# Kernel optimization log

Hardware: AMD Instinct MI355X
Metric: run time of the kernel (lower is better)

The kernel has to match this reference:

```python
import jax, jax.numpy as jnp
import numpy as np

B, T, HID = 2, 2048, 1024
H, D = 16, 64
ROPE = 32
GIDX = (2, 3, 4, 5)
MASK_VAL = -1e9


def setup_inputs() -> dict:
    key = jax.random.key(0)
    ks = jax.random.split(key, 5)
    x = jax.random.normal(ks[0], (B, T, HID), jnp.float32)
    mask = jnp.triu(jnp.ones((T, T), jnp.bool_), 1)  # True above diagonal -> masked (causal)
    qkv_w = jax.random.normal(ks[1], (3 * H * D, HID), jnp.float32) * (1.0 / np.sqrt(HID))
    qkv_b = jax.random.normal(ks[2], (3 * H * D,), jnp.float32) * 0.02
    out_w = jax.random.normal(ks[3], (HID, H * D), jnp.float32) * (1.0 / np.sqrt(H * D))
    out_b = jax.random.normal(ks[4], (HID,), jnp.float32) * 0.02
    return {"x": x, "mask": mask, "qkv_w": qkv_w, "qkv_b": qkv_b, "out_w": out_w, "out_b": out_b}


def _rope_tables(t):
    inv_freq = 1.0 / (10000.0 ** (jnp.arange(0, ROPE, 2, dtype=jnp.float32) / ROPE))
    freqs = jnp.arange(t, dtype=jnp.float32)[:, None] * inv_freq[None, :]  # [T, ROPE/2]
    return jnp.cos(freqs), jnp.sin(freqs)


def _apply_rotary(x, cos, sin):
    # x: [B,H,T,D]; rotate first ROPE dims as interleaved pairs
    xr = x[..., :ROPE].reshape(*x.shape[:-1], ROPE // 2, 2)
    x1, x2 = xr[..., 0], xr[..., 1]
    rot = jnp.stack([x1 * cos - x2 * sin, x1 * sin + x2 * cos], axis=-1).reshape(*x.shape[:-1], ROPE)
    return jnp.concatenate([rot, x[..., ROPE:]], axis=-1)


def reference(x, mask, qkv_w, qkv_b, out_w, out_b):
    b, t, _ = x.shape
    qkv = x @ qkv_w.T + qkv_b                      # [B,T,3*H*D]
    q, k, v = jnp.split(qkv, 3, axis=-1)
    q, k, v = [y.reshape(b, t, H, D).transpose(0, 2, 1, 3) for y in (q, k, v)]  # [B,H,T,D]
    cos, sin = _rope_tables(t)                      # [T, ROPE/2] broadcast over B,H
    q = _apply_rotary(q, cos, sin)
    k = _apply_rotary(k, cos, sin)
    scale = 1.0 / np.sqrt(D)
    # local dense causal attention
    scores = jnp.einsum('bhqd,bhkd->bhqk', q, k) * scale
    scores = jnp.where(mask, MASK_VAL, scores)
    out_local = jnp.einsum('bhqk,bhkd->bhqd', jax.nn.softmax(scores, axis=-1), v)
    # global token pass with its own causal overlay
    gidx = jnp.array(GIDX)
    gq = q[:, :, gidx]                              # [B,H,G,D]
    gs = jnp.einsum('bhgd,bhkd->bhgk', gq, k) * scale
    gmask = jnp.arange(t)[None, :] > gidx[:, None]  # [G,T]: col > row -> masked
    gs = jnp.where(gmask, MASK_VAL, gs)
    gout = jnp.einsum('bhgk,bhkd->bhgd', jax.nn.softmax(gs, axis=-1), v)
    out = out_local.at[:, :, gidx].set(gout)
    attn_out = out.transpose(0, 2, 1, 3).reshape(b, t, H * D)
    return attn_out @ out_w.T + out_b
```

## Files before the change

### kernel.cpp

```cpp
#include <hip/hip_runtime.h>
#include <math.h>

typedef unsigned short u16;
typedef unsigned int u32;
typedef __attribute__((ext_vector_type(4))) float f32x4;
typedef __attribute__((ext_vector_type(8))) short bf16x8;

#define B_ 2
#define T_ 2048
#define H_ 16
#define HID 1024
#define NQKV 3072
#define M_ 4096
#define SCALE_Q 0.18033688011112042f

__device__ __forceinline__ u16 f2bf(float f) {
  union { float f; unsigned u; } v; v.f = f;
  unsigned r = v.u + 0x7FFFu + ((v.u >> 16) & 1u);
  return (u16)(r >> 16);
}
__device__ __forceinline__ float bf2f(u16 u) {
  union { unsigned u; float f; } v; v.u = ((unsigned)u) << 16; return v.f;
}
__device__ __forceinline__ u32 cvt_pk_bf16(float lo, float hi) {
  u32 r;
  asm("v_cvt_pk_bf16_f32 %0, %1, %2" : "=v"(r) : "v"(lo), "v"(hi));
  return r;
}
__device__ __forceinline__ float fexp2(float x) { return __builtin_amdgcn_exp2f(x); }

__device__ __forceinline__ void gload16(const void* g, void* l) {
  __builtin_amdgcn_global_load_lds((const __attribute__((address_space(1))) void*)g,
                                   (__attribute__((address_space(3))) void*)l, 16, 0, 0);
}

__global__ void prep(const float* __restrict__ x, const float* __restrict__ qkv_w,
                     const float* __restrict__ out_w, u16* __restrict__ xb,
                     u16* __restrict__ wqkv, u16* __restrict__ wout, float* __restrict__ tab) {
  int bid = blockIdx.x;
  if (bid < 128) {
    int i = bid * 256 + threadIdx.x;
    int tpos = i >> 4, f = i & 15;
    float ang = (float)tpos * exp2f(-(float)f * 0.83048202372184058696f);
    float s, c;
    sincosf(ang, &s, &c);
    tab[i * 2] = c;
    tab[i * 2 + 1] = s;
    return;
  }
  bid -= 128;
  const float* in;
  u16* out;
  if (bid < 4096) { in = x; out = xb; }
  else if (bid < 7168) { bid -= 4096; in = qkv_w; out = wqkv; }
  else { bid -= 7168; in = out_w; out = wout; }
  int i = bid * 256 + threadIdx.x;
  float4 v = ((const float4*)in)[i];
  uint2 o;
  o.x = (unsigned)f2bf(v.x) | ((unsigned)f2bf(v.y) << 16);
  o.y = (unsigned)f2bf(v.z) | ((unsigned)f2bf(v.w) << 16);
  ((uint2*)out)[i] = o;
}

template<int BM, int WROWS, int OUT_BF16>
__global__ __launch_bounds__(256) void gemm_nt(const u16* __restrict__ A,
    const u16* __restrict__ Bt, const float* __restrict__ bias,
    void* __restrict__ outp, int N, int K)
{
  constexpr int WCOLS = 4 / WROWS;
  constexpr int MI = BM / WROWS / 16;
  constexpr int NI = 128 / WCOLS / 16;
  __shared__ u16 lsA[2][BM * 32];
  __shared__ u16 lsB[2][128 * 32];
  const int t = threadIdx.x;
  const int l = t & 63, w = t >> 6;
  const int wm = (w / WCOLS) * (BM / WROWS);
  const int wn = (w % WCOLS) * (128 / WCOLS);
  const int lr = l & 15, lg = l >> 4;
  const long bm = (long)blockIdx.y * BM, bn = (long)blockIdx.x * 128;

  f32x4 acc[MI][NI];
#pragma unroll
  for (int i = 0; i < MI; i++)
#pragma unroll
    for (int j = 0; j < NI; j++) acc[i][j] = (f32x4){0.f, 0.f, 0.f, 0.f};

  const int srow = l >> 2, sko = (l & 3) * 8;
  const u16* Ab = A + (bm + srow) * (long)K + sko;
  const u16* Bb = Bt + (bn + srow) * (long)K + sko;

  auto stage = [&](int buf, int k0) {
    gload16(Ab + (long)(w * 16) * K + k0, &lsA[buf][w * 512]);
    if constexpr (BM == 128)
      gload16(Ab + (long)((w + 4) * 16) * K + k0, &lsA[buf][(w + 4) * 512]);
    gload16(Bb + (long)(w * 16) * K + k0, &lsB[buf][w * 512]);
    gload16(Bb + (long)((w + 4) * 16) * K + k0, &lsB[buf][(w + 4) * 512]);
  };

  stage(0, 0);
  __syncthreads();
  int cur = 0;
  for (int k0 = 0; k0 < K; k0 += 32) {
    if (k0 + 32 < K) stage(cur ^ 1, k0 + 32);
    bf16x8 af[MI], bfv[NI];
#pragma unroll
    for (int mi = 0; mi < MI; mi++)
      af[mi] = *(const bf16x8*)&lsA[cur][(wm + mi * 16 + lr) * 32 + lg * 8];
#pragma unroll
    for (int ni = 0; ni < NI; ni++)
      bfv[ni] = *(const bf16x8*)&lsB[cur][(wn + ni * 16 + lr) * 32 + lg * 8];
    __builtin_amdgcn_s_setprio(1);
#pragma unroll
    for (int mi = 0; mi < MI; mi++)
#pragma unroll
      for (int ni = 0; ni < NI; ni++)
        acc[mi][ni] = __builtin_amdgcn_mfma_f32_16x16x32_bf16(af[mi], bfv[ni], acc[mi][ni], 0, 0, 0);
    __builtin_amdgcn_s_setprio(0);
    __syncthreads();
    cur ^= 1;
  }
#pragma unroll
  for (int mi = 0; mi < MI; mi++)
#pragma unroll
    for (int ni = 0; ni < NI; ni++) {
      long row = bm + wm + mi * 16 + lg * 4;
      long col = bn + wn + ni * 16 + lr;
      float bv = bias[col];
#pragma unroll
      for (int r = 0; r < 4; r++) {
        float v = acc[mi][ni][r] + bv;
        if (OUT_BF16) ((u16*)outp)[(row + r) * (long)N + col] = f2bf(v);
        else          ((float*)outp)[(row + r) * (long)N + col] = v;
      }
    }
}

__global__ __launch_bounds__(256) void post_qkv(const u16* __restrict__ qkv,
    const float* __restrict__ tab, u16* __restrict__ Q, u16* __restrict__ K,
    u16* __restrict__ Vt) {
  __shared__ u16 ls[64 * 72];
  const int bid = blockIdx.x;
  if (bid < 256) {
    int idx = bid * 256 + threadIdx.x;
    int h = idx & 15;
    int m = idx >> 4;
    int tpos = m & (T_ - 1);
    int b = m >> 11;
    const u16* qr = qkv + (long)m * NQKV + h * 64;
    alignas(16) u16 qv[64];
    alignas(16) u16 kv[64];
#pragma unroll
    for (int c = 0; c < 8; c++) {
      *(int4*)&qv[c * 8] = *(const int4*)&qr[c * 8];
      *(int4*)&kv[c * 8] = *(const int4*)&qr[1024 + c * 8];
    }
#pragma unroll
    for (int i = 0; i < 16; i++) {
      float c = tab[(tpos * 16 + i) * 2];
      float s = tab[(tpos * 16 + i) * 2 + 1];
      float q1 = bf2f(qv[2 * i]), q2 = bf2f(qv[2 * i + 1]);
      qv[2 * i]     = f2bf((q1 * c - q2 * s) * SCALE_Q);
      qv[2 * i + 1] = f2bf((q1 * s + q2 * c) * SCALE_Q);
      float k1 = bf2f(kv[2 * i]), k2 = bf2f(kv[2 * i + 1]);
      kv[2 * i]     = f2bf(k1 * c - k2 * s);
      kv[2 * i + 1] = f2bf(k1 * s + k2 * c);
    }
#pragma unroll
    for (int j = 32; j < 64; j++) qv[j] = f2bf(bf2f(qv[j]) * SCALE_Q);
    long ob = ((long)(b * 16 + h) * T_ + tpos) * 64;
#pragma unroll
    for (int c = 0; c < 8; c++) {
      *(int4*)&Q[ob + c * 8] = *(int4*)&qv[c * 8];
      *(int4*)&K[ob + c * 8] = *(int4*)&kv[c * 8];
    }
  } else {
    int id2 = bid - 256;
    int tt = id2 & 31, bh = id2 >> 5;
    int b = bh >> 4, h = bh & 15;
    int t = threadIdx.x;
    for (int c = t; c < 512; c += 256) {
      int row = c >> 3, off = (c & 7) * 8;
      *(int4*)&ls[row * 72 + off] =
          *(const int4*)&qkv[((long)(b * T_ + tt * 64 + row)) * NQKV + 2048 + h * 64 + off];
    }
    __syncthreads();
    for (int c = t; c < 512; c += 256) {
      int d = c >> 3, toff = (c & 7) * 8;
      alignas(16) u16 tmp[8];
#pragma unroll
      for (int j = 0; j < 8; j++) tmp[j] = ls[(toff + j) * 72 + d];
      *(int4*)&Vt[((long)(bh * 64 + d)) * T_ + tt * 64 + toff] = *(int4*)tmp;
    }
  }
}

__global__ __launch_bounds__(256, 4) void fattn(const u16* __restrict__ Q, const u16* __restrict__ Kp,
                                                const u16* __restrict__ V, u16* __restrict__ O) {
  const int id = blockIdx.x;
  const int qt = 31 - (id >> 5);
  const int bh = id & 31;
  __shared__ u16 lsK[2][64 * 64];
  __shared__ u16 lsV[2][64 * 64];
  __shared__ u32 lsP[4][16 * 36];
  const int t = threadIdx.x, l = t & 63, w = t >> 6;
  const int lr = l & 15, lg = l >> 4;
  const u16* Qb = Q + (long)bh * T_ * 64;
  const u16* Kb = Kp + (long)bh * T_ * 64;
  const u16* Vb = V + (long)bh * 64 * T_;
  u32* lsPw = lsP[w];

  bf16x8 aq[2];
#pragma unroll
  for (int ks = 0; ks < 2; ks++)
    aq[ks] = *(const bf16x8*)&Qb[((long)(qt * 64 + w * 16 + lr)) * 64 + ks * 32 + lg * 8];

  f32x4 o[4];
#pragma unroll
  for (int di = 0; di < 4; di++) o[di] = (f32x4){0.f, 0.f, 0.f, 0.f};
  float mrow = -1e30f, lrow = 0.f;

  const int srow = l >> 3;
  const int scx = ((l & 7) ^ srow) * 8;
  const long kgo0 = (long)(16 * w + srow) * 64 + scx;
  const long kgo1 = (long)(16 * w + 8 + srow) * 64 + scx;
  const long vgo0 = (long)(16 * w + srow) * T_ + scx;
  const long vgo1 = (long)(16 * w + 8 + srow) * T_ + scx;

  gload16(Kb + kgo0, &lsK[0][(2 * w) * 512]);
  gload16(Kb + kgo1, &lsK[0][(2 * w + 1) * 512]);
  gload16(Vb + vgo0, &lsV[0][(2 * w) * 512]);
  gload16(Vb + vgo1, &lsV[0][(2 * w + 1) * 512]);
  __syncthreads();

  int cur = 0;
  for (int kt = 0; kt <= qt; kt++) {
    if (kt < qt) {
      const u16* kp = Kb + (kt + 1) * 4096;
      const u16* vp = Vb + (kt + 1) * 64;
      gload16(kp + kgo0, &lsK[cur ^ 1][(2 * w) * 512]);
      gload16(kp + kgo1, &lsK[cur ^ 1][(2 * w + 1) * 512]);
      gload16(vp + vgo0, &lsV[cur ^ 1][(2 * w) * 512]);
      gload16(vp + vgo1, &lsV[cur ^ 1][(2 * w + 1) * 512]);
    }

    f32x4 s[4];
#pragma unroll
    for (int ji = 0; ji < 4; ji++) s[ji] = (f32x4){0.f, 0.f, 0.f, 0.f};
    __builtin_amdgcn_s_setprio(1);
#pragma unroll
    for (int ks = 0; ks < 2; ks++)
#pragma unroll
      for (int ji = 0; ji < 4; ji++) {
        int row = ji * 16 + lr;
        bf16x8 kf = *(const bf16x8*)&lsK[cur][row * 64 + ((ks * 32 + lg * 8) ^ ((row & 7) * 8))];
        s[ji] = __builtin_amdgcn_mfma_f32_16x16x32_bf16(kf, aq[ks], s[ji], 0, 0, 0);
      }
    __builtin_amdgcn_s_setprio(0);

    if (kt == qt) {
      int qloc = w * 16 + lr;
#pragma unroll
      for (int ji = 0; ji < 4; ji++)
#pragma unroll
        for (int r = 0; r < 4; r++)
          if (ji * 16 + lg * 4 + r > qloc) s[ji][r] = -1e30f;
    }

    float mx = s[0][0];
#pragma unroll
    for (int ji = 0; ji < 4; ji++)
#pragma unroll
      for (int r = 0; r < 4; r++) mx = fmaxf(mx, s[ji][r]);
    mx = fmaxf(mx, __shfl_xor(mx, 16, 64));
    mx = fmaxf(mx, __shfl_xor(mx, 32, 64));

    if (__any(mx - mrow > 8.f)) {
      float newm = fmaxf(mrow, mx);
      float sf = fexp2(mrow - newm);
      mrow = newm;
      lrow *= sf;
#pragma unroll
      for (int r = 0; r < 4; r++) {
        float sfb = __shfl(sf, lg * 4 + r, 64);
#pragma unroll
        for (int di = 0; di < 4; di++) o[di][r] *= sfb;
      }
    }

    float rs = 0.f;
    u32 pd[8];
#pragma unroll
    for (int ji = 0; ji < 4; ji++)
#pragma unroll
      for (int hh = 0; hh < 2; hh++) {
        float p0 = fexp2(s[ji][2 * hh] - mrow);
        float p1 = fexp2(s[ji][2 * hh + 1] - mrow);
        rs += p0 + p1;
        pd[ji * 2 + hh] = cvt_pk_bf16(p0, p1);
      }
    rs += __shfl_xor(rs, 16, 64);
    rs += __shfl_xor(rs, 32, 64);
    lrow += rs;

#pragma unroll
    for (int ji = 0; ji < 4; ji++)
      *(uint2*)&lsPw[lr * 36 + ji * 8 + lg * 2] = make_uint2(pd[2 * ji], pd[2 * ji + 1]);
    __builtin_amdgcn_s_setprio(1);
#pragma unroll
    for (int js = 0; js < 2; js++) {
      bf16x8 pa = *(const bf16x8*)&lsPw[lr * 36 + js * 16 + lg * 4];
#pragma unroll
      for (int di = 0; di < 4; di++) {
        int drow = di * 16 + lr;
        bf16x8 vb = *(const bf16x8*)&lsV[cur][drow * 64 + ((js * 32 + lg * 8) ^ ((drow & 7) * 8))];
        o[di] = __builtin_amdgcn_mfma_f32_16x16x32_bf16(pa, vb, o[di], 0, 0, 0);
      }
    }
    __builtin_amdgcn_s_setprio(0);

    if (kt < qt) __syncthreads();
    cur ^= 1;
  }

  const int b = bh >> 4, h = bh & 15;
  float inv = 1.f / lrow;
#pragma unroll
  for (int r = 0; r < 4; r++) {
    float invb = __shfl(inv, lg * 4 + r, 64);
#pragma unroll
    for (int di = 0; di < 4; di++) {
      long rowt = (long)(b * T_ + qt * 64 + w * 16 + lg * 4 + r);
      O[rowt * 1024 + h * 64 + di * 16 + lr] = f2bf(o[di][r] * invb);
    }
  }
}

extern "C" void kernel_launch(void* const* d_in, const int* in_sizes, int n_in,
                              void* d_out, int out_size, void* d_ws, size_t ws_size,
                              hipStream_t stream) {
  (void)in_sizes; (void)n_in; (void)out_size; (void)ws_size;
  const float* x     = (const float*)d_in[0];
  const float* qkv_w = (const float*)d_in[2];
  const float* qkv_b = (const float*)d_in[3];
  const float* out_w = (const float*)d_in[4];
  const float* out_b = (const float*)d_in[5];
  char* ws = (char*)d_ws;
  size_t off = 0;
  auto alloc = [&](size_t n) { void* p = ws + off; off += (n + 255) & ~(size_t)255; return p; };
  u16*   xb    = (u16*)alloc((size_t)M_ * HID * 2);
  u16*   wqkv  = (u16*)alloc((size_t)NQKV * HID * 2);
  u16*   wout  = (u16*)alloc((size_t)HID * HID * 2);
  u16*   qkvb  = (u16*)alloc((size_t)M_ * NQKV * 2);
  u16*   Qb    = (u16*)alloc((size_t)M_ * HID * 2);
  u16*   Kb    = (u16*)alloc((size_t)M_ * HID * 2);
  u16*   Vtb   = (u16*)alloc((size_t)M_ * HID * 2);
  u16*   attnb = (u16*)alloc((size_t)M_ * HID * 2);
  float* tab   = (float*)alloc((size_t)T_ * 16 * 2 * 4);

  prep<<<8320, 256, 0, stream>>>(x, qkv_w, out_w, xb, wqkv, wout, tab);
  gemm_nt<128, 2, 1><<<dim3(NQKV / 128, M_ / 128), 256, 0, stream>>>(xb, wqkv, qkv_b, qkvb, NQKV, HID);
  post_qkv<<<1280, 256, 0, stream>>>(qkvb, tab, Qb, Kb, Vtb);
  fattn<<<1024, 256, 0, stream>>>(Qb, Kb, Vtb, attnb);
  gemm_nt<64, 1, 0><<<dim3(HID / 128, M_ / 64), 256, 0, stream>>>(attnb, wout, out_b, (float*)d_out, HID, HID);
}
```

Before: 210.7 us.

## Enlarge attention query tile to 128 rows with 8 waves and parametrize GEMM BK

The flash-attention kernel now launches 512-thread blocks, each covering 128 query rows with 8 waves. The waves share each 64-row K/V tile loaded into LDS, which halves the K/V global traffic per query row. Waves whose rows lie entirely before a key tile skip its compute, and the max and sum reductions become tree-shaped. The GEMM gains a BK template parameter: the output projection uses BK=64 with a 128-row tile, cutting barriers per K step, while the QKV GEMM is unchanged. The risks are fewer attention blocks (512) and more causal imbalance inside a block, plus higher LDS and register use.

```diff
diff --git a/kernel.cpp b/kernel.cpp
--- a/kernel.cpp
+++ b/kernel.cpp
@@ -62,7 +62,7 @@
   ((uint2*)out)[i] = o;
 }
 
-template<int BM, int WROWS, int OUT_BF16>
+template<int BM, int BK, int WROWS, int OUT_BF16>
 __global__ __launch_bounds__(256) void gemm_nt(const u16* __restrict__ A,
     const u16* __restrict__ Bt, const float* __restrict__ bias,
     void* __restrict__ outp, int N, int K)
@@ -70,8 +70,11 @@
   constexpr int WCOLS = 4 / WROWS;
   constexpr int MI = BM / WROWS / 16;
   constexpr int NI = 128 / WCOLS / 16;
-  __shared__ u16 lsA[2][BM * 32];
-  __shared__ u16 lsB[2][128 * 32];
+  constexpr int RPG = 512 / BK;
+  constexpr int GA = BM / RPG / 4;
+  constexpr int GB = 128 / RPG / 4;
+  __shared__ u16 lsA[2][BM * BK];
+  __shared__ u16 lsB[2][128 * BK];
   const int t = threadIdx.x;
   const int l = t & 63, w = t >> 6;
   const int wm = (w / WCOLS) * (BM / WROWS);
@@ -85,36 +88,41 @@
 #pragma unroll
     for (int j = 0; j < NI; j++) acc[i][j] = (f32x4){0.f, 0.f, 0.f, 0.f};
 
-  const int srow = l >> 2, sko = (l & 3) * 8;
+  const int srow = l / (BK / 8);
+  const int sko = (l % (BK / 8)) * 8;
   const u16* Ab = A + (bm + srow) * (long)K + sko;
   const u16* Bb = Bt + (bn + srow) * (long)K + sko;
 
   auto stage = [&](int buf, int k0) {
-    gload16(Ab + (long)(w * 16) * K + k0, &lsA[buf][w * 512]);
-    if constexpr (BM == 128)
-      gload16(Ab + (long)((w + 4) * 16) * K + k0, &lsA[buf][(w + 4) * 512]);
-    gload16(Bb + (long)(w * 16) * K + k0, &lsB[buf][w * 512]);
-    gload16(Bb + (long)((w + 4) * 16) * K + k0, &lsB[buf][(w + 4) * 512]);
+#pragma unroll
+    for (int g = 0; g < GA; g++)
+      gload16(Ab + (long)((w * GA + g) * RPG) * K + k0, &lsA[buf][(w * GA + g) * 512]);
+#pragma unroll
+    for (int g = 0; g < GB; g++)
+      gload16(Bb + (long)((w * GB + g) * RPG) * K + k0, &lsB[buf][(w * GB + g) * 512]);
   };
 
   stage(0, 0);
   __syncthreads();
   int cur = 0;
-  for (int k0 = 0; k0 < K; k0 += 32) {
-    if (k0 + 32 < K) stage(cur ^ 1, k0 + 32);
-    bf16x8 af[MI], bfv[NI];
-#pragma unroll
-    for (int mi = 0; mi < MI; mi++)
-      af[mi] = *(const bf16x8*)&lsA[cur][(wm + mi * 16 + lr) * 32 + lg * 8];
-#pragma unroll
-    for (int ni = 0; ni < NI; ni++)
-      bfv[ni] = *(const bf16x8*)&lsB[cur][(wn + ni * 16 + lr) * 32 + lg * 8];
+  for (int k0 = 0; k0 < K; k0 += BK) {
+    if (k0 + BK < K) stage(cur ^ 1, k0 + BK);
     __builtin_amdgcn_s_setprio(1);
 #pragma unroll
-    for (int mi = 0; mi < MI; mi++)
+    for (int kb = 0; kb < BK / 32; kb++) {
+      bf16x8 af[MI], bfv[NI];
+#pragma unroll
+      for (int mi = 0; mi < MI; mi++)
+        af[mi] = *(const bf16x8*)&lsA[cur][(wm + mi * 16 + lr) * BK + kb * 32 + lg * 8];
 #pragma unroll
       for (int ni = 0; ni < NI; ni++)
-        acc[mi][ni] = __builtin_amdgcn_mfma_f32_16x16x32_bf16(af[mi], bfv[ni], acc[mi][ni], 0, 0, 0);
+        bfv[ni] = *(const bf16x8*)&lsB[cur][(wn + ni * 16 + lr) * BK + kb * 32 + lg * 8];
+#pragma unroll
+      for (int mi = 0; mi < MI; mi++)
+#pragma unroll
+        for (int ni = 0; ni < NI; ni++)
+          acc[mi][ni] = __builtin_amdgcn_mfma_f32_16x16x32_bf16(af[mi], bfv[ni], acc[mi][ni], 0, 0, 0);
+    }
     __builtin_amdgcn_s_setprio(0);
     __syncthreads();
     cur ^= 1;
@@ -194,25 +202,27 @@
   }
 }
 
-__global__ __launch_bounds__(256, 4) void fattn(const u16* __restrict__ Q, const u16* __restrict__ Kp,
+__global__ __launch_bounds__(512, 4) void fattn(const u16* __restrict__ Q, const u16* __restrict__ Kp,
                                                 const u16* __restrict__ V, u16* __restrict__ O) {
   const int id = blockIdx.x;
-  const int qt = 31 - (id >> 5);
+  const int qs = 15 - (id >> 5);
   const int bh = id & 31;
   __shared__ u16 lsK[2][64 * 64];
   __shared__ u16 lsV[2][64 * 64];
-  __shared__ u32 lsP[4][16 * 36];
+  __shared__ u32 lsP[8][16 * 36];
   const int t = threadIdx.x, l = t & 63, w = t >> 6;
   const int lr = l & 15, lg = l >> 4;
   const u16* Qb = Q + (long)bh * T_ * 64;
   const u16* Kb = Kp + (long)bh * T_ * 64;
   const u16* Vb = V + (long)bh * 64 * T_;
   u32* lsPw = lsP[w];
+  const int qbase = qs * 128 + w * 16;
+  const int qg = qbase + lr;
 
   bf16x8 aq[2];
 #pragma unroll
   for (int ks = 0; ks < 2; ks++)
-    aq[ks] = *(const bf16x8*)&Qb[((long)(qt * 64 + w * 16 + lr)) * 64 + ks * 32 + lg * 8];
+    aq[ks] = *(const bf16x8*)&Qb[(long)qg * 64 + ks * 32 + lg * 8];
 
   f32x4 o[4];
 #pragma unroll
@@ -221,104 +231,103 @@
 
   const int srow = l >> 3;
   const int scx = ((l & 7) ^ srow) * 8;
-  const long kgo0 = (long)(16 * w + srow) * 64 + scx;
-  const long kgo1 = (long)(16 * w + 8 + srow) * 64 + scx;
-  const long vgo0 = (long)(16 * w + srow) * T_ + scx;
-  const long vgo1 = (long)(16 * w + 8 + srow) * T_ + scx;
-
-  gload16(Kb + kgo0, &lsK[0][(2 * w) * 512]);
-  gload16(Kb + kgo1, &lsK[0][(2 * w + 1) * 512]);
-  gload16(Vb + vgo0, &lsV[0][(2 * w) * 512]);
-  gload16(Vb + vgo1, &lsV[0][(2 * w + 1) * 512]);
+  const long kgo = (long)(8 * w + srow) * 64 + scx;
+  const long vgo = (long)(8 * w + srow) * T_ + scx;
+
+  gload16(Kb + kgo, &lsK[0][w * 512]);
+  gload16(Vb + vgo, &lsV[0][w * 512]);
   __syncthreads();
 
   int cur = 0;
-  for (int kt = 0; kt <= qt; kt++) {
-    if (kt < qt) {
-      const u16* kp = Kb + (kt + 1) * 4096;
-      const u16* vp = Vb + (kt + 1) * 64;
-      gload16(kp + kgo0, &lsK[cur ^ 1][(2 * w) * 512]);
-      gload16(kp + kgo1, &lsK[cur ^ 1][(2 * w + 1) * 512]);
-      gload16(vp + vgo0, &lsV[cur ^ 1][(2 * w) * 512]);
-      gload16(vp + vgo1, &lsV[cur ^ 1][(2 * w + 1) * 512]);
-    }
-
-    f32x4 s[4];
-#pragma unroll
-    for (int ji = 0; ji < 4; ji++) s[ji] = (f32x4){0.f, 0.f, 0.f, 0.f};
-    __builtin_amdgcn_s_setprio(1);
-#pragma unroll
-    for (int ks = 0; ks < 2; ks++)
-#pragma unroll
-      for (int ji = 0; ji < 4; ji++) {
-        int row = ji * 16 + lr;
-        bf16x8 kf = *(const bf16x8*)&lsK[cur][row * 64 + ((ks * 32 + lg * 8) ^ ((row & 7) * 8))];
-        s[ji] = __builtin_amdgcn_mfma_f32_16x16x32_bf16(kf, aq[ks], s[ji], 0, 0, 0);
-      }
-    __builtin_amdgcn_s_setprio(0);
-
-    if (kt == qt) {
-      int qloc = w * 16 + lr;
+  const int ktmax = 2 * qs + 1;
+  for (int kt = 0; kt <= ktmax; kt++) {
+    if (kt < ktmax) {
+      gload16(Kb + (long)(kt + 1) * 4096 + kgo, &lsK[cur ^ 1][w * 512]);
+      gload16(Vb + (long)(kt + 1) * 64 + vgo, &lsV[cur ^ 1][w * 512]);
+    }
+    const int kbase = kt * 64;
+    if (kbase <= qbase + 15) {
+      f32x4 s[4];
+#pragma unroll
+      for (int ji = 0; ji < 4; ji++) s[ji] = (f32x4){0.f, 0.f, 0.f, 0.f};
+      __builtin_amdgcn_s_setprio(1);
+#pragma unroll
+      for (int ks = 0; ks < 2; ks++)
+#pragma unroll
+        for (int ji = 0; ji < 4; ji++) {
+          int row = ji * 16 + lr;
+          bf16x8 kf = *(const bf16x8*)&lsK[cur][row * 64 + ((ks * 32 + lg * 8) ^ ((row & 7) * 8))];
+          s[ji] = __builtin_amdgcn_mfma_f32_16x16x32_bf16(kf, aq[ks], s[ji], 0, 0, 0);
+        }
+      __builtin_amdgcn_s_setprio(0);
+
+      if (kbase + 63 > qbase) {
+#pragma unroll
+        for (int ji = 0; ji < 4; ji++)
+#pragma unroll
+          for (int r = 0; r < 4; r++)
+            if (kbase + ji * 16 + lg * 4 + r > qg) s[ji][r] = -1e30f;
+      }
+
+      float m01 = fmaxf(fmaxf(s[0][0], s[0][1]), fmaxf(s[0][2], s[0][3]));
+      float m23 = fmaxf(fmaxf(s[1][0], s[1][1]), fmaxf(s[1][2], s[1][3]));
+      float m45 = fmaxf(fmaxf(s[2][0], s[2][1]), fmaxf(s[2][2], s[2][3]));
+      float m67 = fmaxf(fmaxf(s[3][0], s[3][1]), fmaxf(s[3][2], s[3][3]));
+      float mx = fmaxf(fmaxf(m01, m23), fmaxf(m45, m67));
+      mx = fmaxf(mx, __shfl_xor(mx, 16, 64));
+      mx = fmaxf(mx, __shfl_xor(mx, 32, 64));
+
+      if (__any(mx - mrow > 8.f)) {
+        float newm = fmaxf(mrow, mx);
+        float sf = fexp2(mrow - newm);
+        mrow = newm;
+        lrow *= sf;
+#pragma unroll
+        for (int r = 0; r < 4; r++) {
+          float sfb = __shfl(sf, lg * 4 + r, 64);
+#pragma unroll
+          for (int di = 0; di < 4; di++) o[di][r] *= sfb;
+        }
+      }
+
+      float p[16];
+      u32 pd[8];
 #pragma unroll
       for (int ji = 0; ji < 4; ji++)
 #pragma unroll
-        for (int r = 0; r < 4; r++)
-          if (ji * 16 + lg * 4 + r > qloc) s[ji][r] = -1e30f;
-    }
-
-    float mx = s[0][0];
-#pragma unroll
-    for (int ji = 0; ji < 4; ji++)
-#pragma unroll
-      for (int r = 0; r < 4; r++) mx = fmaxf(mx, s[ji][r]);
-    mx = fmaxf(mx, __shfl_xor(mx, 16, 64));
-    mx = fmaxf(mx, __shfl_xor(mx, 32, 64));
-
-    if (__any(mx - mrow > 8.f)) {
-      float newm = fmaxf(mrow, mx);
-      float sf = fexp2(mrow - newm);
-      mrow = newm;
-      lrow *= sf;
-#pragma unroll
-      for (int r = 0; r < 4; r++) {
-        float sfb = __shfl(sf, lg * 4 + r, 64);
-#pragma unroll
-        for (int di = 0; di < 4; di++) o[di][r] *= sfb;
-      }
-    }
-
-    float rs = 0.f;
-    u32 pd[8];
-#pragma unroll
-    for (int ji = 0; ji < 4; ji++)
-#pragma unroll
-      for (int hh = 0; hh < 2; hh++) {
-        float p0 = fexp2(s[ji][2 * hh] - mrow);
-        float p1 = fexp2(s[ji][2 * hh + 1] - mrow);
-        rs += p0 + p1;
-        pd[ji * 2 + hh] = cvt_pk_bf16(p0, p1);
-      }
-    rs += __shfl_xor(rs, 16, 64);
-    rs += __shfl_xor(rs, 32, 64);
-    lrow += rs;
-
-#pragma unroll
-    for (int ji = 0; ji < 4; ji++)
-      *(uint2*)&lsPw[lr * 36 + ji * 8 + lg * 2] = make_uint2(pd[2 * ji], pd[2 * ji + 1]);
-    __builtin_amdgcn_s_setprio(1);
-#pragma unroll
-    for (int js = 0; js < 2; js++) {
-      bf16x8 pa = *(const bf16x8*)&lsPw[lr * 36 + js * 16 + lg * 4];
-#pragma unroll
-      for (int di = 0; di < 4; di++) {
-        int drow = di * 16 + lr;
-        bf16x8 vb = *(const bf16x8*)&lsV[cur][drow * 64 + ((js * 32 + lg * 8) ^ ((drow & 7) * 8))];
-        o[di] = __builtin_amdgcn_mfma_f32_16x16x32_bf16(pa, vb, o[di], 0, 0, 0);
-      }
-    }
-    __builtin_amdgcn_s_setprio(0);
-
-    if (kt < qt) __syncthreads();
+        for (int r = 0; r < 4; r++) p[ji * 4 + r] = fexp2(s[ji][r] - mrow);
+#pragma unroll
+      for (int jj = 0; jj < 8; jj++) pd[jj] = cvt_pk_bf16(p[2 * jj], p[2 * jj + 1]);
+      float rs = 0.f;
+      {
+        float a0 = (p[0] + p[1]) + (p[2] + p[3]);
+        float a1 = (p[4] + p[5]) + (p[6] + p[7]);
+        float a2 = (p[8] + p[9]) + (p[10] + p[11]);
+        float a3 = (p[12] + p[13]) + (p[14] + p[15]);
+        rs = (a0 + a1) + (a2 + a3);
+      }
+      rs += __shfl_xor(rs, 16, 64);
+      rs += __shfl_xor(rs, 32, 64);
+      lrow += rs;
+
+#pragma unroll
+      for (int ji = 0; ji < 4; ji++)
+        *(uint2*)&lsPw[lr * 36 + ji * 8 + lg * 2] = make_uint2(pd[2 * ji], pd[2 * ji + 1]);
+      __builtin_amdgcn_s_setprio(1);
+#pragma unroll
+      for (int js = 0; js < 2; js++) {
+        bf16x8 pa = *(const bf16x8*)&lsPw[lr * 36 + js * 16 + lg * 4];
+#pragma unroll
+        for (int di = 0; di < 4; di++) {
+          int drow = di * 16 + lr;
+          bf16x8 vb = *(const bf16x8*)&lsV[cur][drow * 64 + ((js * 32 + lg * 8) ^ ((drow & 7) * 8))];
+          o[di] = __builtin_amdgcn_mfma_f32_16x16x32_bf16(pa, vb, o[di], 0, 0, 0);
+        }
+      }
+      __builtin_amdgcn_s_setprio(0);
+    }
+
+    if (kt < ktmax) __syncthreads();
     cur ^= 1;
   }
 
@@ -329,7 +338,7 @@
     float invb = __shfl(inv, lg * 4 + r, 64);
 #pragma unroll
     for (int di = 0; di < 4; di++) {
-      long rowt = (long)(b * T_ + qt * 64 + w * 16 + lg * 4 + r);
+      long rowt = (long)(b * T_ + qbase + lg * 4 + r);
       O[rowt * 1024 + h * 64 + di * 16 + lr] = f2bf(o[di][r] * invb);
     }
   }
@@ -358,8 +367,8 @@
   float* tab   = (float*)alloc((size_t)T_ * 16 * 2 * 4);
 
   prep<<<8320, 256, 0, stream>>>(x, qkv_w, out_w, xb, wqkv, wout, tab);
-  gemm_nt<128, 2, 1><<<dim3(NQKV / 128, M_ / 128), 256, 0, stream>>>(xb, wqkv, qkv_b, qkvb, NQKV, HID);
+  gemm_nt<128, 32, 2, 1><<<dim3(NQKV / 128, M_ / 128), 256, 0, stream>>>(xb, wqkv, qkv_b, qkvb, NQKV, HID);
   post_qkv<<<1280, 256, 0, stream>>>(qkvb, tab, Qb, Kb, Vtb);
-  fattn<<<1024, 256, 0, stream>>>(Qb, Kb, Vtb, attnb);
-  gemm_nt<64, 1, 0><<<dim3(HID / 128, M_ / 64), 256, 0, stream>>>(attnb, wout, out_b, (float*)d_out, HID, HID);
-}
+  fattn<<<512, 512, 0, stream>>>(Qb, Kb, Vtb, attnb);
+  gemm_nt<128, 64, 2, 0><<<dim3(HID / 128, M_ / 128), 256, 0, stream>>>(attnb, wout, out_b, (float*)d_out, HID, HID);
+}
```

Measured after the change: 220.5 us. 4.6% more time.

## Double query rows per attention wave and enlarge QKV GEMM tile

Applied to the files above, without the earlier changes.

The flash attention kernel now gives each wave 32 query rows (two 16-row groups) over a 128-row query block. Each K/V tile loaded into shared memory therefore feeds twice as many MFMAs, and the grid is halved. Fully masked key tiles are skipped per wave, and occupancy is lowered to 3 blocks. Separately, the QKV GEMM uses a 256-row M tile with generalized staging loops and launch bounds of 2, which raises register pressure and reduces block count.

```diff
diff --git a/kernel.cpp b/kernel.cpp
--- a/kernel.cpp
+++ b/kernel.cpp
@@ -63,13 +63,15 @@
 }
 
 template<int BM, int WROWS, int OUT_BF16>
-__global__ __launch_bounds__(256) void gemm_nt(const u16* __restrict__ A,
+__global__ __launch_bounds__(256, 2) void gemm_nt(const u16* __restrict__ A,
     const u16* __restrict__ Bt, const float* __restrict__ bias,
     void* __restrict__ outp, int N, int K)
 {
   constexpr int WCOLS = 4 / WROWS;
   constexpr int MI = BM / WROWS / 16;
   constexpr int NI = 128 / WCOLS / 16;
+  constexpr int GA = BM / 16 / 4;
+  constexpr int GB = 128 / 16 / 4;
   __shared__ u16 lsA[2][BM * 32];
   __shared__ u16 lsB[2][128 * 32];
   const int t = threadIdx.x;
@@ -90,11 +92,12 @@
   const u16* Bb = Bt + (bn + srow) * (long)K + sko;
 
   auto stage = [&](int buf, int k0) {
-    gload16(Ab + (long)(w * 16) * K + k0, &lsA[buf][w * 512]);
-    if constexpr (BM == 128)
-      gload16(Ab + (long)((w + 4) * 16) * K + k0, &lsA[buf][(w + 4) * 512]);
-    gload16(Bb + (long)(w * 16) * K + k0, &lsB[buf][w * 512]);
-    gload16(Bb + (long)((w + 4) * 16) * K + k0, &lsB[buf][(w + 4) * 512]);
+#pragma unroll
+    for (int g = 0; g < GA; g++)
+      gload16(Ab + (long)((w * GA + g) * 16) * K + k0, &lsA[buf][(w * GA + g) * 512]);
+#pragma unroll
+    for (int g = 0; g < GB; g++)
+      gload16(Bb + (long)((w * GB + g) * 16) * K + k0, &lsB[buf][(w * GB + g) * 512]);
   };
 
   stage(0, 0);
@@ -194,30 +197,35 @@
   }
 }
 
-__global__ __launch_bounds__(256, 4) void fattn(const u16* __restrict__ Q, const u16* __restrict__ Kp,
+__global__ __launch_bounds__(256, 3) void fattn(const u16* __restrict__ Q, const u16* __restrict__ Kp,
                                                 const u16* __restrict__ V, u16* __restrict__ O) {
   const int id = blockIdx.x;
-  const int qt = 31 - (id >> 5);
+  const int qs = 15 - (id >> 5);
   const int bh = id & 31;
   __shared__ u16 lsK[2][64 * 64];
   __shared__ u16 lsV[2][64 * 64];
-  __shared__ u32 lsP[4][16 * 36];
+  __shared__ u32 lsP[4][32 * 36];
   const int t = threadIdx.x, l = t & 63, w = t >> 6;
   const int lr = l & 15, lg = l >> 4;
   const u16* Qb = Q + (long)bh * T_ * 64;
   const u16* Kb = Kp + (long)bh * T_ * 64;
   const u16* Vb = V + (long)bh * 64 * T_;
   u32* lsPw = lsP[w];
-
-  bf16x8 aq[2];
-#pragma unroll
-  for (int ks = 0; ks < 2; ks++)
-    aq[ks] = *(const bf16x8*)&Qb[((long)(qt * 64 + w * 16 + lr)) * 64 + ks * 32 + lg * 8];
-
-  f32x4 o[4];
-#pragma unroll
-  for (int di = 0; di < 4; di++) o[di] = (f32x4){0.f, 0.f, 0.f, 0.f};
-  float mrow = -1e30f, lrow = 0.f;
+  const int qbase = qs * 128 + w * 32;
+
+  bf16x8 aq[2][2];
+#pragma unroll
+  for (int qg = 0; qg < 2; qg++)
+#pragma unroll
+    for (int ks = 0; ks < 2; ks++)
+      aq[qg][ks] = *(const bf16x8*)&Qb[((long)(qbase + qg * 16 + lr)) * 64 + ks * 32 + lg * 8];
+
+  f32x4 o[2][4];
+#pragma unroll
+  for (int qg = 0; qg < 2; qg++)
+#pragma unroll
+    for (int di = 0; di < 4; di++) o[qg][di] = (f32x4){0.f, 0.f, 0.f, 0.f};
+  float mrow[2] = {-1e30f, -1e30f}, lrow[2] = {0.f, 0.f};
 
   const int srow = l >> 3;
   const int scx = ((l & 7) ^ srow) * 8;
@@ -233,8 +241,9 @@
   __syncthreads();
 
   int cur = 0;
-  for (int kt = 0; kt <= qt; kt++) {
-    if (kt < qt) {
+  const int ktmax = 2 * qs + 1;
+  for (int kt = 0; kt <= ktmax; kt++) {
+    if (kt < ktmax) {
       const u16* kp = Kb + (kt + 1) * 4096;
       const u16* vp = Vb + (kt + 1) * 64;
       gload16(kp + kgo0, &lsK[cur ^ 1][(2 * w) * 512]);
@@ -242,95 +251,114 @@
       gload16(vp + vgo0, &lsV[cur ^ 1][(2 * w) * 512]);
       gload16(vp + vgo1, &lsV[cur ^ 1][(2 * w + 1) * 512]);
     }
-
-    f32x4 s[4];
-#pragma unroll
-    for (int ji = 0; ji < 4; ji++) s[ji] = (f32x4){0.f, 0.f, 0.f, 0.f};
-    __builtin_amdgcn_s_setprio(1);
-#pragma unroll
-    for (int ks = 0; ks < 2; ks++)
-#pragma unroll
-      for (int ji = 0; ji < 4; ji++) {
-        int row = ji * 16 + lr;
-        bf16x8 kf = *(const bf16x8*)&lsK[cur][row * 64 + ((ks * 32 + lg * 8) ^ ((row & 7) * 8))];
-        s[ji] = __builtin_amdgcn_mfma_f32_16x16x32_bf16(kf, aq[ks], s[ji], 0, 0, 0);
+    const int kbase = kt * 64;
+    if (kbase <= qbase + 31) {
+      f32x4 s[2][4];
+#pragma unroll
+      for (int qg = 0; qg < 2; qg++)
+#pragma unroll
+        for (int ji = 0; ji < 4; ji++) s[qg][ji] = (f32x4){0.f, 0.f, 0.f, 0.f};
+      __builtin_amdgcn_s_setprio(1);
+#pragma unroll
+      for (int ks = 0; ks < 2; ks++)
+#pragma unroll
+        for (int ji = 0; ji < 4; ji++) {
+          int row = ji * 16 + lr;
+          bf16x8 kf = *(const bf16x8*)&lsK[cur][row * 64 + ((ks * 32 + lg * 8) ^ ((row & 7) * 8))];
+          s[0][ji] = __builtin_amdgcn_mfma_f32_16x16x32_bf16(kf, aq[0][ks], s[0][ji], 0, 0, 0);
+          s[1][ji] = __builtin_amdgcn_mfma_f32_16x16x32_bf16(kf, aq[1][ks], s[1][ji], 0, 0, 0);
+        }
+      __builtin_amdgcn_s_setprio(0);
+
+#pragma unroll
+      for (int qg = 0; qg < 2; qg++) {
+        const int qg_q = qbase + qg * 16 + lr;
+        if (kbase + 63 > qbase + qg * 16) {
+#pragma unroll
+          for (int ji = 0; ji < 4; ji++)
+#pragma unroll
+            for (int r = 0; r < 4; r++)
+              if (kbase + ji * 16 + lg * 4 + r > qg_q) s[qg][ji][r] = -1e30f;
+        }
+
+        float m01 = fmaxf(fmaxf(s[qg][0][0], s[qg][0][1]), fmaxf(s[qg][0][2], s[qg][0][3]));
+        float m23 = fmaxf(fmaxf(s[qg][1][0], s[qg][1][1]), fmaxf(s[qg][1][2], s[qg][1][3]));
+        float m45 = fmaxf(fmaxf(s[qg][2][0], s[qg][2][1]), fmaxf(s[qg][2][2], s[qg][2][3]));
+        float m67 = fmaxf(fmaxf(s[qg][3][0], s[qg][3][1]), fmaxf(s[qg][3][2], s[qg][3][3]));
+        float mx = fmaxf(fmaxf(m01, m23), fmaxf(m45, m67));
+        mx = fmaxf(mx, __shfl_xor(mx, 16, 64));
+        mx = fmaxf(mx, __shfl_xor(mx, 32, 64));
+
+        if (__any(mx - mrow[qg] > 8.f)) {
+          float newm = fmaxf(mrow[qg], mx);
+          float sf = fexp2(mrow[qg] - newm);
+          mrow[qg] = newm;
+          lrow[qg] *= sf;
+#pragma unroll
+          for (int r = 0; r < 4; r++) {
+            float sfb = __shfl(sf, lg * 4 + r, 64);
+#pragma unroll
+            for (int di = 0; di < 4; di++) o[qg][di][r] *= sfb;
+          }
+        }
+
+        float p[16];
+        u32 pd[8];
+#pragma unroll
+        for (int ji = 0; ji < 4; ji++)
+#pragma unroll
+          for (int r = 0; r < 4; r++) p[ji * 4 + r] = fexp2(s[qg][ji][r] - mrow[qg]);
+#pragma unroll
+        for (int jj = 0; jj < 8; jj++) pd[jj] = cvt_pk_bf16(p[2 * jj], p[2 * jj + 1]);
+        float rs;
+        {
+          float a0 = (p[0] + p[1]) + (p[2] + p[3]);
+          float a1 = (p[4] + p[5]) + (p[6] + p[7]);
+          float a2 = (p[8] + p[9]) + (p[10] + p[11]);
+          float a3 = (p[12] + p[13]) + (p[14] + p[15]);
+          rs = (a0 + a1) + (a2 + a3);
+        }
+        rs += __shfl_xor(rs, 16, 64);
+        rs += __shfl_xor(rs, 32, 64);
+        lrow[qg] += rs;
+
+#pragma unroll
+        for (int ji = 0; ji < 4; ji++)
+          *(uint2*)&lsPw[(qg * 16 + lr) * 36 + ji * 8 + lg * 2] = make_uint2(pd[2 * ji], pd[2 * ji + 1]);
       }
-    __builtin_amdgcn_s_setprio(0);
-
-    if (kt == qt) {
-      int qloc = w * 16 + lr;
-#pragma unroll
-      for (int ji = 0; ji < 4; ji++)
-#pragma unroll
-        for (int r = 0; r < 4; r++)
-          if (ji * 16 + lg * 4 + r > qloc) s[ji][r] = -1e30f;
-    }
-
-    float mx = s[0][0];
-#pragma unroll
-    for (int ji = 0; ji < 4; ji++)
-#pragma unroll
-      for (int r = 0; r < 4; r++) mx = fmaxf(mx, s[ji][r]);
-    mx = fmaxf(mx, __shfl_xor(mx, 16, 64));
-    mx = fmaxf(mx, __shfl_xor(mx, 32, 64));
-
-    if (__any(mx - mrow > 8.f)) {
-      float newm = fmaxf(mrow, mx);
-      float sf = fexp2(mrow - newm);
-      mrow = newm;
-      lrow *= sf;
-#pragma unroll
-      for (int r = 0; r < 4; r++) {
-        float sfb = __shfl(sf, lg * 4 + r, 64);
-#pragma unroll
-        for (int di = 0; di < 4; di++) o[di][r] *= sfb;
+
+      __builtin_amdgcn_s_setprio(1);
+#pragma unroll
+      for (int js = 0; js < 2; js++) {
+        bf16x8 pa0 = *(const bf16x8*)&lsPw[lr * 36 + js * 16 + lg * 4];
+        bf16x8 pa1 = *(const bf16x8*)&lsPw[(16 + lr) * 36 + js * 16 + lg * 4];
+#pragma unroll
+        for (int di = 0; di < 4; di++) {
+          int drow = di * 16 + lr;
+          bf16x8 vb = *(const bf16x8*)&lsV[cur][drow * 64 + ((js * 32 + lg * 8) ^ ((drow & 7) * 8))];
+          o[0][di] = __builtin_amdgcn_mfma_f32_16x16x32_bf16(pa0, vb, o[0][di], 0, 0, 0);
+          o[1][di] = __builtin_amdgcn_mfma_f32_16x16x32_bf16(pa1, vb, o[1][di], 0, 0, 0);
+        }
       }
-    }
-
-    float rs = 0.f;
-    u32 pd[8];
-#pragma unroll
-    for (int ji = 0; ji < 4; ji++)
-#pragma unroll
-      for (int hh = 0; hh < 2; hh++) {
-        float p0 = fexp2(s[ji][2 * hh] - mrow);
-        float p1 = fexp2(s[ji][2 * hh + 1] - mrow);
-        rs += p0 + p1;
-        pd[ji * 2 + hh] = cvt_pk_bf16(p0, p1);
+      __builtin_amdgcn_s_setprio(0);
+    }
+
+    if (kt < ktmax) __syncthreads();
+    cur ^= 1;
+  }
+
+  const int b = bh >> 4, h = bh & 15;
+#pragma unroll
+  for (int qg = 0; qg < 2; qg++) {
+    float inv = 1.f / lrow[qg];
+#pragma unroll
+    for (int r = 0; r < 4; r++) {
+      float invb = __shfl(inv, lg * 4 + r, 64);
+#pragma unroll
+      for (int di = 0; di < 4; di++) {
+        long rowt = (long)(b * T_ + qbase + qg * 16 + lg * 4 + r);
+        O[rowt * 1024 + h * 64 + di * 16 + lr] = f2bf(o[qg][di][r] * invb);
       }
-    rs += __shfl_xor(rs, 16, 64);
-    rs += __shfl_xor(rs, 32, 64);
-    lrow += rs;
-
-#pragma unroll
-    for (int ji = 0; ji < 4; ji++)
-      *(uint2*)&lsPw[lr * 36 + ji * 8 + lg * 2] = make_uint2(pd[2 * ji], pd[2 * ji + 1]);
-    __builtin_amdgcn_s_setprio(1);
-#pragma unroll
-    for (int js = 0; js < 2; js++) {
-      bf16x8 pa = *(const bf16x8*)&lsPw[lr * 36 + js * 16 + lg * 4];
-#pragma unroll
-      for (int di = 0; di < 4; di++) {
-        int drow = di * 16 + lr;
-        bf16x8 vb = *(const bf16x8*)&lsV[cur][drow * 64 + ((js * 32 + lg * 8) ^ ((drow & 7) * 8))];
-        o[di] = __builtin_amdgcn_mfma_f32_16x16x32_bf16(pa, vb, o[di], 0, 0, 0);
-      }
-    }
-    __builtin_amdgcn_s_setprio(0);
-
-    if (kt < qt) __syncthreads();
-    cur ^= 1;
-  }
-
-  const int b = bh >> 4, h = bh & 15;
-  float inv = 1.f / lrow;
-#pragma unroll
-  for (int r = 0; r < 4; r++) {
-    float invb = __shfl(inv, lg * 4 + r, 64);
-#pragma unroll
-    for (int di = 0; di < 4; di++) {
-      long rowt = (long)(b * T_ + qt * 64 + w * 16 + lg * 4 + r);
-      O[rowt * 1024 + h * 64 + di * 16 + lr] = f2bf(o[di][r] * invb);
     }
   }
 }
@@ -358,8 +386,8 @@
   float* tab   = (float*)alloc((size_t)T_ * 16 * 2 * 4);
 
   prep<<<8320, 256, 0, stream>>>(x, qkv_w, out_w, xb, wqkv, wout, tab);
-  gemm_nt<128, 2, 1><<<dim3(NQKV / 128, M_ / 128), 256, 0, stream>>>(xb, wqkv, qkv_b, qkvb, NQKV, HID);
+  gemm_nt<256, 2, 1><<<dim3(NQKV / 128, M_ / 256), 256, 0, stream>>>(xb, wqkv, qkv_b, qkvb, NQKV, HID);
   post_qkv<<<1280, 256, 0, stream>>>(qkvb, tab, Qb, Kb, Vtb);
-  fattn<<<1024, 256, 0, stream>>>(Qb, Kb, Vtb, attnb);
+  fattn<<<512, 256, 0, stream>>>(Qb, Kb, Vtb, attnb);
   gemm_nt<64, 1, 0><<<dim3(HID / 128, M_ / 64), 256, 0, stream>>>(attnb, wout, out_b, (float*)d_out, HID, HID);
 }
```

Result: slower. 229.0 us (+8.7%).

## Fuse RoPE, Q scaling and head-split/V-transpose into QKV GEMM epilogue

Applied to the files above, without the earlier changes.

The QKV GEMM epilogue now applies bias, rotary embedding (pairing lanes through a shuffle), the Q scale and the per-head layout scatter itself. It writes Q, K and transposed V directly and drops the intermediate qkv buffer and the post_qkv kernel. This removes one kernel launch and a full round trip of the 4096x3072 bf16 intermediate through global memory. In exchange the epilogue stores are scattered 2-byte writes for Q/K and strided 8-byte writes for V, where the removed kernel used 16-byte vector stores. The output GEMM is specialized into a non-templated kernel with the same tiling.

```diff
diff --git a/kernel.cpp b/kernel.cpp
--- a/kernel.cpp
+++ b/kernel.cpp
@@ -62,20 +62,118 @@
   ((uint2*)out)[i] = o;
 }
 
-template<int BM, int WROWS, int OUT_BF16>
-__global__ __launch_bounds__(256) void gemm_nt(const u16* __restrict__ A,
+__global__ __launch_bounds__(256) void gemm_qkv(const u16* __restrict__ A,
+    const u16* __restrict__ Bt, const float* __restrict__ bias, const float* __restrict__ tab,
+    u16* __restrict__ Q, u16* __restrict__ K, u16* __restrict__ Vt)
+{
+  __shared__ u16 lsA[2][128 * 32];
+  __shared__ u16 lsB[2][128 * 32];
+  const int t = threadIdx.x;
+  const int l = t & 63, w = t >> 6;
+  const int wm = (w >> 1) * 64, wn = (w & 1) * 64;
+  const int lr = l & 15, lg = l >> 4;
+  const long bm = (long)blockIdx.y * 128, bn = (long)blockIdx.x * 128;
+  const int KD = HID;
+
+  f32x4 acc[4][4];
+#pragma unroll
+  for (int i = 0; i < 4; i++)
+#pragma unroll
+    for (int j = 0; j < 4; j++) acc[i][j] = (f32x4){0.f, 0.f, 0.f, 0.f};
+
+  const int srow = l >> 2, sko = (l & 3) * 8;
+  const u16* Ab = A + (bm + srow) * (long)KD + sko;
+  const u16* Bb = Bt + (bn + srow) * (long)KD + sko;
+
+  auto stage = [&](int buf, int k0) {
+#pragma unroll
+    for (int g = 0; g < 2; g++)
+      gload16(Ab + (long)((w * 2 + g) * 16) * KD + k0, &lsA[buf][(w * 2 + g) * 512]);
+#pragma unroll
+    for (int g = 0; g < 2; g++)
+      gload16(Bb + (long)((w * 2 + g) * 16) * KD + k0, &lsB[buf][(w * 2 + g) * 512]);
+  };
+
+  stage(0, 0);
+  __syncthreads();
+  int cur = 0;
+  for (int k0 = 0; k0 < KD; k0 += 32) {
+    if (k0 + 32 < KD) stage(cur ^ 1, k0 + 32);
+    bf16x8 af[4], bfv[4];
+#pragma unroll
+    for (int mi = 0; mi < 4; mi++)
+      af[mi] = *(const bf16x8*)&lsA[cur][(wm + mi * 16 + lr) * 32 + lg * 8];
+#pragma unroll
+    for (int ni = 0; ni < 4; ni++)
+      bfv[ni] = *(const bf16x8*)&lsB[cur][(wn + ni * 16 + lr) * 32 + lg * 8];
+    __builtin_amdgcn_s_setprio(1);
+#pragma unroll
+    for (int mi = 0; mi < 4; mi++)
+#pragma unroll
+      for (int ni = 0; ni < 4; ni++)
+        acc[mi][ni] = __builtin_amdgcn_mfma_f32_16x16x32_bf16(af[mi], bfv[ni], acc[mi][ni], 0, 0, 0);
+    __builtin_amdgcn_s_setprio(0);
+    __syncthreads();
+    cur ^= 1;
+  }
+
+  const int region = (int)(bn >> 10);
+  const int h = (int)(((bn + wn) & 1023) >> 6);
+  const float2* tab2 = (const float2*)tab;
+  u16* QK = (region == 0) ? Q : K;
+
+#pragma unroll
+  for (int mi = 0; mi < 4; mi++) {
+    const int m0 = (int)(bm) + wm + mi * 16 + lg * 4;
+    const int b = m0 >> 11, t0 = m0 & (T_ - 1);
+    const long bh = b * 16 + h;
+#pragma unroll
+    for (int ni = 0; ni < 4; ni++) {
+      const int d = ni * 16 + lr;
+      const long col = bn + wn + d;
+      const float bv = bias[col];
+      float vv[4];
+#pragma unroll
+      for (int r = 0; r < 4; r++) vv[r] = acc[mi][ni][r] + bv;
+      if (region < 2 && ni < 2) {
+        const int fi = d >> 1;
+        const float sgn = (d & 1) ? 1.f : -1.f;
+#pragma unroll
+        for (int r = 0; r < 4; r++) {
+          float pvv = __shfl_xor(vv[r], 1, 64);
+          float2 cs = tab2[(t0 + r) * 16 + fi];
+          vv[r] = vv[r] * cs.x + sgn * pvv * cs.y;
+        }
+      }
+      if (region == 0) {
+#pragma unroll
+        for (int r = 0; r < 4; r++) vv[r] *= SCALE_Q;
+      }
+      if (region < 2) {
+#pragma unroll
+        for (int r = 0; r < 4; r++)
+          QK[(bh * T_ + t0 + r) * 64 + d] = f2bf(vv[r]);
+      } else {
+        uint2 pk;
+        pk.x = cvt_pk_bf16(vv[0], vv[1]);
+        pk.y = cvt_pk_bf16(vv[2], vv[3]);
+        *(uint2*)&Vt[(bh * 64 + d) * (long)T_ + t0] = pk;
+      }
+    }
+  }
+}
+
+__global__ __launch_bounds__(256) void gemm_out(const u16* __restrict__ A,
     const u16* __restrict__ Bt, const float* __restrict__ bias,
-    void* __restrict__ outp, int N, int K)
+    float* __restrict__ outp, int N, int K)
 {
-  constexpr int WCOLS = 4 / WROWS;
-  constexpr int MI = BM / WROWS / 16;
-  constexpr int NI = 128 / WCOLS / 16;
+  constexpr int BM = 64;
+  constexpr int MI = 4, NI = 2;
   __shared__ u16 lsA[2][BM * 32];
   __shared__ u16 lsB[2][128 * 32];
   const int t = threadIdx.x;
   const int l = t & 63, w = t >> 6;
-  const int wm = (w / WCOLS) * (BM / WROWS);
-  const int wn = (w % WCOLS) * (128 / WCOLS);
+  const int wn = w * 32;
   const int lr = l & 15, lg = l >> 4;
   const long bm = (long)blockIdx.y * BM, bn = (long)blockIdx.x * 128;
 
@@ -91,8 +189,6 @@
 
   auto stage = [&](int buf, int k0) {
     gload16(Ab + (long)(w * 16) * K + k0, &lsA[buf][w * 512]);
-    if constexpr (BM == 128)
-      gload16(Ab + (long)((w + 4) * 16) * K + k0, &lsA[buf][(w + 4) * 512]);
     gload16(Bb + (long)(w * 16) * K + k0, &lsB[buf][w * 512]);
     gload16(Bb + (long)((w + 4) * 16) * K + k0, &lsB[buf][(w + 4) * 512]);
   };
@@ -105,7 +201,7 @@
     bf16x8 af[MI], bfv[NI];
 #pragma unroll
     for (int mi = 0; mi < MI; mi++)
-      af[mi] = *(const bf16x8*)&lsA[cur][(wm + mi * 16 + lr) * 32 + lg * 8];
+      af[mi] = *(const bf16x8*)&lsA[cur][(mi * 16 + lr) * 32 + lg * 8];
 #pragma unroll
     for (int ni = 0; ni < NI; ni++)
       bfv[ni] = *(const bf16x8*)&lsB[cur][(wn + ni * 16 + lr) * 32 + lg * 8];
@@ -123,75 +219,13 @@
   for (int mi = 0; mi < MI; mi++)
 #pragma unroll
     for (int ni = 0; ni < NI; ni++) {
-      long row = bm + wm + mi * 16 + lg * 4;
+      long row = bm + mi * 16 + lg * 4;
       long col = bn + wn + ni * 16 + lr;
       float bv = bias[col];
 #pragma unroll
-      for (int r = 0; r < 4; r++) {
-        float v = acc[mi][ni][r] + bv;
-        if (OUT_BF16) ((u16*)outp)[(row + r) * (long)N + col] = f2bf(v);
-        else          ((float*)outp)[(row + r) * (long)N + col] = v;
-      }
-    }
-}
-
-__global__ __launch_bounds__(256) void post_qkv(const u16* __restrict__ qkv,
-    const float* __restrict__ tab, u16* __restrict__ Q, u16* __restrict__ K,
-    u16* __restrict__ Vt) {
-  __shared__ u16 ls[64 * 72];
-  const int bid = blockIdx.x;
-  if (bid < 256) {
-    int idx = bid * 256 + threadIdx.x;
-    int h = idx & 15;
-    int m = idx >> 4;
-    int tpos = m & (T_ - 1);
-    int b = m >> 11;
-    const u16* qr = qkv + (long)m * NQKV + h * 64;
-    alignas(16) u16 qv[64];
-    alignas(16) u16 kv[64];
-#pragma unroll
-    for (int c = 0; c < 8; c++) {
-      *(int4*)&qv[c * 8] = *(const int4*)&qr[c * 8];
-      *(int4*)&kv[c * 8] = *(const int4*)&qr[1024 + c * 8];
-    }
-#pragma unroll
-    for (int i = 0; i < 16; i++) {
-      float c = tab[(tpos * 16 + i) * 2];
-      float s = tab[(tpos * 16 + i) * 2 + 1];
-      float q1 = bf2f(qv[2 * i]), q2 = bf2f(qv[2 * i + 1]);
-      qv[2 * i]     = f2bf((q1 * c - q2 * s) * SCALE_Q);
-      qv[2 * i + 1] = f2bf((q1 * s + q2 * c) * SCALE_Q);
-      float k1 = bf2f(kv[2 * i]), k2 = bf2f(kv[2 * i + 1]);
-      kv[2 * i]     = f2bf(k1 * c - k2 * s);
-      kv[2 * i + 1] = f2bf(k1 * s + k2 * c);
-    }
-#pragma unroll
-    for (int j = 32; j < 64; j++) qv[j] = f2bf(bf2f(qv[j]) * SCALE_Q);
-    long ob = ((long)(b * 16 + h) * T_ + tpos) * 64;
-#pragma unroll
-    for (int c = 0; c < 8; c++) {
-      *(int4*)&Q[ob + c * 8] = *(int4*)&qv[c * 8];
-      *(int4*)&K[ob + c * 8] = *(int4*)&kv[c * 8];
-    }
-  } else {
-    int id2 = bid - 256;
-    int tt = id2 & 31, bh = id2 >> 5;
-    int b = bh >> 4, h = bh & 15;
-    int t = threadIdx.x;
-    for (int c = t; c < 512; c += 256) {
-      int row = c >> 3, off = (c & 7) * 8;
-      *(int4*)&ls[row * 72 + off] =
-          *(const int4*)&qkv[((long)(b * T_ + tt * 64 + row)) * NQKV + 2048 + h * 64 + off];
-    }
-    __syncthreads();
-    for (int c = t; c < 512; c += 256) {
-      int d = c >> 3, toff = (c & 7) * 8;
-      alignas(16) u16 tmp[8];
-#pragma unroll
-      for (int j = 0; j < 8; j++) tmp[j] = ls[(toff + j) * 72 + d];
-      *(int4*)&Vt[((long)(bh * 64 + d)) * T_ + tt * 64 + toff] = *(int4*)tmp;
-    }
-  }
+      for (int r = 0; r < 4; r++)
+        outp[(row + r) * (long)N + col] = acc[mi][ni][r] + bv;
+    }
 }
 
 __global__ __launch_bounds__(256, 4) void fattn(const u16* __restrict__ Q, const u16* __restrict__ Kp,
@@ -350,7 +384,6 @@
   u16*   xb    = (u16*)alloc((size_t)M_ * HID * 2);
   u16*   wqkv  = (u16*)alloc((size_t)NQKV * HID * 2);
   u16*   wout  = (u16*)alloc((size_t)HID * HID * 2);
-  u16*   qkvb  = (u16*)alloc((size_t)M_ * NQKV * 2);
   u16*   Qb    = (u16*)alloc((size_t)M_ * HID * 2);
   u16*   Kb    = (u16*)alloc((size_t)M_ * HID * 2);
   u16*   Vtb   = (u16*)alloc((size_t)M_ * HID * 2);
@@ -358,8 +391,7 @@
   float* tab   = (float*)alloc((size_t)T_ * 16 * 2 * 4);
 
   prep<<<8320, 256, 0, stream>>>(x, qkv_w, out_w, xb, wqkv, wout, tab);
-  gemm_nt<128, 2, 1><<<dim3(NQKV / 128, M_ / 128), 256, 0, stream>>>(xb, wqkv, qkv_b, qkvb, NQKV, HID);
-  post_qkv<<<1280, 256, 0, stream>>>(qkvb, tab, Qb, Kb, Vtb);
+  gemm_qkv<<<dim3(NQKV / 128, M_ / 128), 256, 0, stream>>>(xb, wqkv, qkv_b, tab, Qb, Kb, Vtb);
   fattn<<<1024, 256, 0, stream>>>(Qb, Kb, Vtb, attnb);
-  gemm_nt<64, 1, 0><<<dim3(HID / 128, M_ / 64), 256, 0, stream>>>(attnb, wout, out_b, (float*)d_out, HID, HID);
-}
+  gemm_out<<<dim3(HID / 128, M_ / 64), 256, 0, stream>>>(attnb, wout, out_b, (float*)d_out, HID, HID);
+}
```

Result: faster. 194.3 us (-7.8%).
